# Kernel optimization log

Measured on AMD Instinct MI355X. Metric: run time of the kernel, lower is better.

## Reference

```python
import jax, jax.numpy as jnp
import numpy as np

H = 256  # hidden_size


def _lstm_layer(x, W_ih, W_hh, b_ih, b_hh):
    """Single LSTM layer, batch_first input x: [B, T, I]. PyTorch gate order i,f,g,o."""
    # Precompute input contribution for all timesteps: [B, T, 4H]
    gx = jnp.einsum('bti,gi->btg', x, W_ih) + (b_ih + b_hh)
    gx = jnp.swapaxes(gx, 0, 1)  # [T, B, 4H]
    B = x.shape[0]
    h0 = jnp.zeros((B, H), dtype=x.dtype)
    c0 = jnp.zeros((B, H), dtype=x.dtype)

    def step(carry, g_t):
        h, c = carry
        g = g_t + h @ W_hh.T  # [B, 4H]
        i, f, gg, o = jnp.split(g, 4, axis=-1)
        i = jax.nn.sigmoid(i)
        f = jax.nn.sigmoid(f)
        gg = jnp.tanh(gg)
        o = jax.nn.sigmoid(o)
        c_new = f * c + i * gg
        h_new = o * jnp.tanh(c_new)
        return (h_new, c_new), h_new

    _, hs = jax.lax.scan(step, (h0, c0), gx)  # hs: [T, B, H]
    return jnp.swapaxes(hs, 0, 1)  # [B, T, H]


def setup_inputs() -> dict:
    key = jax.random.key(0)
    ks = jax.random.split(key, 12)
    B, T, I = 512, 256, 10
    s_in = 1.0 / np.sqrt(H)
    inp = {
        'x': jax.random.normal(ks[0], (B, T, I), dtype=jnp.float32),
        # layer 0: input_size=10
        'W_ih0': jax.random.uniform(ks[1], (4 * H, I), jnp.float32, -s_in, s_in),
        'W_hh0': jax.random.uniform(ks[2], (4 * H, H), jnp.float32, -s_in, s_in),
        'b_ih0': jax.random.uniform(ks[3], (4 * H,), jnp.float32, -s_in, s_in),
        'b_hh0': jax.random.uniform(ks[4], (4 * H,), jnp.float32, -s_in, s_in),
        # layer 1: input_size=H
        'W_ih1': jax.random.uniform(ks[5], (4 * H, H), jnp.float32, -s_in, s_in),
        'W_hh1': jax.random.uniform(ks[6], (4 * H, H), jnp.float32, -s_in, s_in),
        'b_ih1': jax.random.uniform(ks[7], (4 * H,), jnp.float32, -s_in, s_in),
        'b_hh1': jax.random.uniform(ks[8], (4 * H,), jnp.float32, -s_in, s_in),
        # final linear head: hidden_size -> 1
        'W_lin': jax.random.uniform(ks[9], (1, H), jnp.float32, -s_in, s_in),
        'b_lin': jax.random.uniform(ks[10], (1,), jnp.float32, -s_in, s_in),
    }
    return inp


def reference(x, W_ih0, W_hh0, b_ih0, b_hh0, W_ih1, W_hh1, b_ih1, b_hh1, W_lin, b_lin):
    h1 = _lstm_layer(x, W_ih0, W_hh0, b_ih0, b_hh0)   # [B, T, H]
    h2 = _lstm_layer(h1, W_ih1, W_hh1, b_ih1, b_hh1)  # [B, T, H]
    y = h2[:, -1, :] @ W_lin.T + b_lin                # [B, 1]
    return y
```

## Files before the change

kernel.cpp:

```cpp
#include <hip/hip_runtime.h>
#include <math.h>

typedef unsigned int u32;
typedef unsigned long long u64;
typedef __attribute__((ext_vector_type(8))) short bf16x8;
typedef __attribute__((ext_vector_type(4))) float f32x4;
typedef __attribute__((ext_vector_type(4))) int i32x4;

#define TT 256

#define BOFF_WT   0ULL
#define BOFF_WX   3932160ULL
#define BOFF_H0HI 3973120ULL
#define BOFF_H0LO 4497408ULL
#define BOFF_H1HI 5021696ULL
#define BOFF_H1LO 5545984ULL
#define BOFF_FLG  6070272ULL

#define OB_H0HI 3973120u
#define OB_H0LO 4497408u
#define OB_H1HI 5021696u
#define OB_H1LO 5545984u
#define OB_FLGF 6070272u
#define OB_FLGS 6074368u

__global__ void transpose_gi(const float* __restrict__ W, float* __restrict__ A, int K) {
    int idx = blockIdx.x * 256 + threadIdx.x;
    if (idx < K * 1024) {
        int kk = idx >> 10, r = idx & 1023, k = r >> 2, g = r & 3;
        A[idx] = W[(g * 256 + k) * K + kk];
    }
}

__global__ void split_w(const float* __restrict__ W0, const float* __restrict__ W1,
                        const float* __restrict__ W2, unsigned short* __restrict__ wt) {
    int idx = blockIdx.x * 256 + threadIdx.x;
    int k32 = idx & 31;
    int n   = (idx >> 5) & 1023;
    int kc  = (idx >> 15) & 7;
    int mt  = idx >> 18;
    const float* W = (mt == 0) ? W0 : (mt == 1) ? W1 : W2;
    int ug = n >> 2, g = n & 3, k = kc * 32 + k32;
    float v = W[(g * 256 + ug) * 256 + k];
    u32 b = __float_as_uint(v);
    unsigned short hi = (unsigned short)(b >> 16);
    float lo = v - __uint_as_float(b & 0xFFFF0000u);
    u32 lb = __float_as_uint(lo);
    unsigned short los = (unsigned short)((lb + 0x7FFFu + ((lb >> 16) & 1u)) >> 16);
    wt[((size_t)((mt * 2 + 0) * 8 + kc) * 1024 + n) * 40 + k32] = hi;
    wt[((size_t)((mt * 2 + 1) * 8 + kc) * 1024 + n) * 40 + k32] = los;
}

__device__ __forceinline__ float sigf(float x)     { return 1.0f / (1.0f + __expf(-x)); }
__device__ __forceinline__ float tanhfast(float x) { return 1.0f - 2.0f / (__expf(2.0f * x) + 1.0f); }

__device__ __forceinline__ unsigned short bhi(float v) {
    return (unsigned short)(__float_as_uint(v) >> 16);
}
__device__ __forceinline__ unsigned short blo(float v) {
    float lo = v - __uint_as_float(__float_as_uint(v) & 0xFFFF0000u);
    u32 lb = __float_as_uint(lo);
    return (unsigned short)((lb + 0x7FFFu + ((lb >> 16) & 1u)) >> 16);
}
__device__ __forceinline__ float bff(u32 us) { return __uint_as_float(us << 16); }

__device__ __forceinline__ i32x4 mksrd(const void* p) {
    u64 a = (u64)p;
    i32x4 r;
    r.x = (int)(u32)a;
    r.y = (int)((a >> 32) & 0xFFFFu);
    r.z = (int)0xFFFFFFFFu;
    r.w = 0x00020000;
    return r;
}

#define WAITV(N) do { asm volatile("s_waitcnt vmcnt(" #N ")" ::: "memory"); \
                      __builtin_amdgcn_sched_barrier(0); } while (0)

__device__ __forceinline__ void ld16s(bf16x8& d, i32x4 rs, u32 voff) {
    asm volatile("buffer_load_dwordx4 %0, %1, %2, 0 offen sc0"
                 : "=v"(d) : "v"(voff), "s"(rs));
}
__device__ __forceinline__ void st4s(i32x4 rs, u32 voff, u32 v) {
    asm volatile("buffer_store_dword %0, %1, %2, 0 offen sc0"
                 :: "v"(v), "v"(voff), "s"(rs) : "memory");
}
__device__ __forceinline__ u32 ld4s(i32x4 rs, u32 voff) {
    u32 d;
    asm volatile("buffer_load_dword %0, %1, %2, 0 offen sc0"
                 : "=v"(d) : "v"(voff), "s"(rs) : "memory");
    return d;
}
__device__ __forceinline__ u32 mkrdy_fast(i32x4 rs, u32 flB, int lane, u32 tgt) {
    u32 v;
    u32 off = flB + (u32)((lane & 31) * 4);
    asm volatile("buffer_load_dword %0, %1, %2, 0 offen sc0\n\t"
                 "s_waitcnt vmcnt(0)"
                 : "=v"(v) : "v"(off), "s"(rs) : "memory");
    unsigned long long b = __ballot(v >= tgt);
    return (u32)b;
}
__device__ __forceinline__ u32 mkrdy_safe(const u32* fl, int lane, u32 tgt) {
    u32 v = __hip_atomic_load(fl + (lane & 31), __ATOMIC_RELAXED,
                              __HIP_MEMORY_SCOPE_AGENT);
    unsigned long long b = __ballot(v >= tgt);
    return (u32)b;
}

__global__ __launch_bounds__(256, 1)
void lstm_mfma(const float* __restrict__ x,
               const float* __restrict__ bih0, const float* __restrict__ bhh0,
               const float* __restrict__ bih1, const float* __restrict__ bhh1,
               const float* __restrict__ Wlin, const float* __restrict__ blin,
               char* __restrict__ wsb, float* __restrict__ out)
{
    __shared__ unsigned short lw[61440];
    __shared__ float fsh[5184];
    float* ldsWx = fsh;
    float* xs    = fsh + 320;
    float* CS    = fsh + 960;

    const int tid  = threadIdx.x;
    const int lane = tid & 63;
    const int wv   = __builtin_amdgcn_readfirstlane(tid >> 6);
    const int quad = lane >> 4;
    const int l15  = lane & 15;
    const int ib   = blockIdx.x & 7;
    const int ik   = blockIdx.x >> 3;
    const int rb0  = ib * 64;

    i32x4 rs = mksrd(wsb);

    const unsigned short* wt = (const unsigned short*)(wsb + BOFF_WT);
    const float* gWx = (const float*)(wsb + BOFF_WX);
    const u32 flF  = OB_FLGF + (u32)(ib * 128);
    const u32* flS = (const u32*)(wsb + OB_FLGS) + ib * 32;
    u32* flSw      = (u32*)(wsb + OB_FLGS) + ib * 32 + ik;

    #pragma unroll 1
    for (int j = 0; j < 30; ++j) {
        int i16 = tid + j * 256;
        int chk = i16 / 160;
        int wi  = i16 - chk * 160;
        size_t src = (size_t)chk * 40960 + (size_t)ik * 1280 + (size_t)wi * 8;
        *(ulonglong2*)(lw + (size_t)chk * 1280 + (size_t)wi * 8) =
            *(const ulonglong2*)(wt + src);
    }
    for (int n = tid; n < 320; n += 256)
        ldsWx[n] = gWx[(n >> 5) * 1024 + ik * 32 + (n & 31)];

    float b0r[8], b1r[8];
    {
        int up = tid & 3;
        #pragma unroll
        for (int j = 0; j < 8; ++j) {
            int ul = up * 2 + (j >> 2), g = j & 3;
            int gi = g * 256 + ik * 8 + ul;
            b0r[j] = bih0[gi] + bhh0[gi];
            b1r[j] = bih1[gi] + bhh1[gi];
        }
    }
    float c0s[2] = {0.f, 0.f}, c1s[2] = {0.f, 0.f};
    const u32 oaB = (u32)(quad * 1024 + (wv * 16 + l15) * 16);
    const bf16x8* bw = (const bf16x8*)lw;
    int safeMode = 0;

    __syncthreads();

    for (int e = 0; e <= TT; ++e) {
        {
            int te = (e < TT) ? e : (TT - 1);
            #pragma unroll
            for (int rr = 0; rr < 2; ++rr) {
                int idx = tid + rr * 256;
                if (idx < 320) {
                    int r = idx / 5, j2 = idx - r * 5;
                    float2 v = *(const float2*)(x + (size_t)(rb0 + r) * 2560 + te * 10 + 2 * j2);
                    xs[(2 * j2) * 64 + r]     = v.x;
                    xs[(2 * j2 + 1) * 64 + r] = v.y;
                }
            }
        }
        __syncthreads();

        {
            const u32 tgt = (u32)e;
            u32 rdy;
            if (!safeMode) {
                rdy = mkrdy_fast(rs, flF, lane, tgt);
                int sp = 0;
                while (rdy != 0xFFFFFFFFu && ++sp < 4096)
                    rdy = mkrdy_fast(rs, flF, lane, tgt);
                if (rdy != 0xFFFFFFFFu) safeMode = 1;
            }
            if (safeMode) {
                rdy = mkrdy_safe(flS, lane, tgt);
                while (rdy != 0xFFFFFFFFu) {
                    __builtin_amdgcn_s_sleep(2);
                    rdy = mkrdy_safe(flS, lane, tgt);
                }
            }
            __builtin_amdgcn_sched_barrier(0);
        }
        WAITV(0);

        const u32 vo0 = OB_H0HI + (u32)((((e + 1) & 1) * 8 + ib) * 32768);
        const u32 vo1 = OB_H0LO + (u32)((((e + 1) & 1) * 8 + ib) * 32768);
        const u32 vo2 = OB_H1HI + (u32)(((e & 1) * 8 + ib) * 32768);
        const u32 vo3 = OB_H1LO + (u32)(((e & 1) * 8 + ib) * 32768);

        bf16x8 fA[2][4];
        #define ISSUE(b, qc) { const u32 tB = (u32)((qc) * 4096) + oaB;   \
            ld16s(fA[b][0], rs, vo0 + tB);                                \
            ld16s(fA[b][1], rs, vo1 + tB);                                \
            ld16s(fA[b][2], rs, vo2 + tB);                                \
            ld16s(fA[b][3], rs, vo3 + tB); }
        ISSUE(0, 0)
        ISSUE(1, 1)

        float xc[8];
        {
            int r = tid >> 2, up = tid & 3;
            #pragma unroll
            for (int j = 0; j < 8; ++j) xc[j] = b0r[j];
            #pragma unroll
            for (int i = 0; i < 10; ++i) {
                float xv = xs[i * 64 + r];
                #pragma unroll
                for (int j = 0; j < 8; ++j)
                    xc[j] += xv * ldsWx[i * 32 + up * 8 + j];
            }
        }

        f32x4 C0[2], C1[2];
        #pragma unroll
        for (int ct = 0; ct < 2; ++ct) {
            C0[ct] = (f32x4){0.f, 0.f, 0.f, 0.f};
            C1[ct] = (f32x4){0.f, 0.f, 0.f, 0.f};
        }

        #pragma unroll
        for (int q = 0; q < 8; ++q) {
            const int b = q & 1;
            bf16x8 wA[2][2], wB[2][2], wC[2][2];
            #pragma unroll
            for (int ct = 0; ct < 2; ++ct) {
                int rb = ct * 16 + l15;
                wA[0][ct] = bw[5 * ((0 * 8 + q) * 32 + rb) + quad];
                wA[1][ct] = bw[5 * ((1 * 8 + q) * 32 + rb) + quad];
                wB[0][ct] = bw[5 * ((2 * 8 + q) * 32 + rb) + quad];
                wB[1][ct] = bw[5 * ((3 * 8 + q) * 32 + rb) + quad];
                wC[0][ct] = bw[5 * ((4 * 8 + q) * 32 + rb) + quad];
                wC[1][ct] = bw[5 * ((5 * 8 + q) * 32 + rb) + quad];
            }
            if (q < 7) { WAITV(4); } else { WAITV(0); }
            bf16x8 a0h = fA[b][0], a0l = fA[b][1];
            bf16x8 a1h = fA[b][2], a1l = fA[b][3];
            #pragma unroll
            for (int ct = 0; ct < 2; ++ct) {
                C0[ct] = __builtin_amdgcn_mfma_f32_16x16x32_bf16(a0h, wA[0][ct], C0[ct], 0, 0, 0);
                C0[ct] = __builtin_amdgcn_mfma_f32_16x16x32_bf16(a0h, wA[1][ct], C0[ct], 0, 0, 0);
                C0[ct] = __builtin_amdgcn_mfma_f32_16x16x32_bf16(a0l, wA[0][ct], C0[ct], 0, 0, 0);
                C0[ct] = __builtin_amdgcn_mfma_f32_16x16x32_bf16(a0l, wA[1][ct], C0[ct], 0, 0, 0);
                C1[ct] = __builtin_amdgcn_mfma_f32_16x16x32_bf16(a0h, wB[0][ct], C1[ct], 0, 0, 0);
                C1[ct] = __builtin_amdgcn_mfma_f32_16x16x32_bf16(a0h, wB[1][ct], C1[ct], 0, 0, 0);
                C1[ct] = __builtin_amdgcn_mfma_f32_16x16x32_bf16(a0l, wB[0][ct], C1[ct], 0, 0, 0);
                C1[ct] = __builtin_amdgcn_mfma_f32_16x16x32_bf16(a0l, wB[1][ct], C1[ct], 0, 0, 0);
                C1[ct] = __builtin_amdgcn_mfma_f32_16x16x32_bf16(a1h, wC[0][ct], C1[ct], 0, 0, 0);
                C1[ct] = __builtin_amdgcn_mfma_f32_16x16x32_bf16(a1h, wC[1][ct], C1[ct], 0, 0, 0);
                C1[ct] = __builtin_amdgcn_mfma_f32_16x16x32_bf16(a1l, wC[0][ct], C1[ct], 0, 0, 0);
                C1[ct] = __builtin_amdgcn_mfma_f32_16x16x32_bf16(a1l, wC[1][ct], C1[ct], 0, 0, 0);
            }
            if (q < 6) ISSUE(b, q + 2)
        }
        #undef ISSUE

        #pragma unroll
        for (int ct = 0; ct < 2; ++ct)
            #pragma unroll
            for (int reg = 0; reg < 4; ++reg) {
                int rr = wv * 16 + quad * 4 + reg;
                CS[rr * 33 + ct * 16 + l15]        = C0[ct][reg];
                CS[2112 + rr * 33 + ct * 16 + l15] = C1[ct][reg];
            }
        __syncthreads();

        {
            int r = tid >> 2, up = tid & 3;
            if (e < TT) {
                float h0n[2];
                #pragma unroll
                for (int s = 0; s < 2; ++s) {
                    int c4 = up * 8 + s * 4;
                    float gi = CS[r * 33 + c4 + 0] + xc[s * 4 + 0];
                    float gf = CS[r * 33 + c4 + 1] + xc[s * 4 + 1];
                    float gg = CS[r * 33 + c4 + 2] + xc[s * 4 + 2];
                    float go = CS[r * 33 + c4 + 3] + xc[s * 4 + 3];
                    float cn = sigf(gf) * c0s[s] + sigf(gi) * tanhfast(gg);
                    c0s[s] = cn;
                    h0n[s] = sigf(go) * tanhfast(cn);
                }
                u32 sb = (u32)(((e & 1) * 8 + ib) * 32768 + ik * 1024 + 4 * tid);
                st4s(rs, OB_H0HI + sb, (u32)bhi(h0n[0]) | ((u32)bhi(h0n[1]) << 16));
                st4s(rs, OB_H0LO + sb, (u32)blo(h0n[0]) | ((u32)blo(h0n[1]) << 16));
            }
            if (e > 0) {
                float h1n[2];
                #pragma unroll
                for (int s = 0; s < 2; ++s) {
                    int c4 = up * 8 + s * 4;
                    float gi = CS[2112 + r * 33 + c4 + 0] + b1r[s * 4 + 0];
                    float gf = CS[2112 + r * 33 + c4 + 1] + b1r[s * 4 + 1];
                    float gg = CS[2112 + r * 33 + c4 + 2] + b1r[s * 4 + 2];
                    float go = CS[2112 + r * 33 + c4 + 3] + b1r[s * 4 + 3];
                    float cn = sigf(gf) * c1s[s] + sigf(gi) * tanhfast(gg);
                    c1s[s] = cn;
                    h1n[s] = sigf(go) * tanhfast(cn);
                }
                u32 sb = (u32)((((e + 1) & 1) * 8 + ib) * 32768 + ik * 1024 + 4 * tid);
                st4s(rs, OB_H1HI + sb, (u32)bhi(h1n[0]) | ((u32)bhi(h1n[1]) << 16));
                st4s(rs, OB_H1LO + sb, (u32)blo(h1n[0]) | ((u32)blo(h1n[1]) << 16));
            }
        }
        WAITV(0);
        __syncthreads();
        if (tid == 0) {
            st4s(rs, flF + (u32)(ik * 4), (u32)(e + 1));
            __hip_atomic_store(flSw, (u32)(e + 1),
                               __ATOMIC_RELAXED, __HIP_MEMORY_SCOPE_AGENT);
        }
    }

    if (ik == 0) {
        {
            const u32 tgt = (u32)(TT + 1);
            u32 rdy;
            if (!safeMode) {
                rdy = mkrdy_fast(rs, flF, lane, tgt);
                int sp = 0;
                while (rdy != 0xFFFFFFFFu && ++sp < 4096)
                    rdy = mkrdy_fast(rs, flF, lane, tgt);
                if (rdy != 0xFFFFFFFFu) safeMode = 1;
            }
            if (safeMode) {
                rdy = mkrdy_safe(flS, lane, tgt);
                while (rdy != 0xFFFFFFFFu) {
                    __builtin_amdgcn_s_sleep(2);
                    rdy = mkrdy_safe(flS, lane, tgt);
                }
            }
            __builtin_amdgcn_sched_barrier(0);
        }
        int r = tid >> 2, q4 = tid & 3;
        const u32 bh_ = OB_H1HI + (u32)((8 + ib) * 32768);
        const u32 bl_ = OB_H1LO + (u32)((8 + ib) * 32768);
        float sacc = 0.f;
        #pragma unroll 1
        for (int kk = 0; kk < 64; kk += 8) {
            u32 hw4[4], lw4[4];
            #pragma unroll
            for (int t = 0; t < 4; ++t) {
                int k = q4 * 64 + kk + 2 * t;
                u32 sa = (u32)(((k >> 3) * 512 + r * 8 + (k & 7)) * 2);
                hw4[t] = ld4s(rs, bh_ + sa);
                lw4[t] = ld4s(rs, bl_ + sa);
            }
            WAITV(0);
            #pragma unroll
            for (int t = 0; t < 4; ++t) {
                int k = q4 * 64 + kk + 2 * t;
                sacc += (bff(hw4[t] & 0xFFFFu) + bff(lw4[t] & 0xFFFFu)) * Wlin[k];
                sacc += (bff(hw4[t] >> 16)     + bff(lw4[t] >> 16))     * Wlin[k + 1];
            }
        }
        sacc += __shfl_down(sacc, 2, 4);
        sacc += __shfl_down(sacc, 1, 4);
        if (q4 == 0) out[rb0 + r] = sacc + blin[0];
    }
}

extern "C" void kernel_launch(void* const* d_in, const int* in_sizes, int n_in,
                              void* d_out, int out_size, void* d_ws, size_t ws_size,
                              hipStream_t stream) {
    const float* x     = (const float*)d_in[0];
    const float* W_ih0 = (const float*)d_in[1];
    const float* W_hh0 = (const float*)d_in[2];
    const float* b_ih0 = (const float*)d_in[3];
    const float* b_hh0 = (const float*)d_in[4];
    const float* W_ih1 = (const float*)d_in[5];
    const float* W_hh1 = (const float*)d_in[6];
    const float* b_ih1 = (const float*)d_in[7];
    const float* b_hh1 = (const float*)d_in[8];
    const float* W_lin = (const float*)d_in[9];
    const float* b_lin = (const float*)d_in[10];
    float* out = (float*)d_out;
    char* wsb  = (char*)d_ws;

    hipMemsetAsync(wsb + BOFF_H0HI, 0, 4 * 524288 + 131584, stream);

    split_w<<<3072, 256, 0, stream>>>(W_hh0, W_ih1, W_hh1,
                                      (unsigned short*)(wsb + BOFF_WT));
    transpose_gi<<<40, 256, 0, stream>>>(W_ih0, (float*)(wsb + BOFF_WX), 10);

    lstm_mfma<<<256, 256, 0, stream>>>(x, b_ih0, b_hh0, b_ih1, b_hh1,
                                       W_lin, b_lin, wsb, out);
}
```

Before: 1.546 ms.

## Wait on per-chunk producer readiness bits instead of a full-step barrier

Replaces the single wait for all 32 producer flags at the start of each timestep with incremental waits. Each chunk of the hidden-state K dimension waits only on the flag bits of the blocks that produce that chunk, just before its loads are issued. This lets the MFMA work on early chunks overlap with producers that are still finishing the later chunks. It adds repeated flag polling inside the inner loop and changes the spin limit and sleep interval, which could add overhead or contention.

```diff
diff --git a/kernel.cpp b/kernel.cpp
--- a/kernel.cpp
+++ b/kernel.cpp
@@ -182,27 +182,30 @@
             }
         }
         __syncthreads();
-
-        {
-            const u32 tgt = (u32)e;
-            u32 rdy;
-            if (!safeMode) {
-                rdy = mkrdy_fast(rs, flF, lane, tgt);
-                int sp = 0;
-                while (rdy != 0xFFFFFFFFu && ++sp < 4096)
-                    rdy = mkrdy_fast(rs, flF, lane, tgt);
-                if (rdy != 0xFFFFFFFFu) safeMode = 1;
-            }
-            if (safeMode) {
-                rdy = mkrdy_safe(flS, lane, tgt);
-                while (rdy != 0xFFFFFFFFu) {
-                    __builtin_amdgcn_s_sleep(2);
-                    rdy = mkrdy_safe(flS, lane, tgt);
-                }
-            }
-            __builtin_amdgcn_sched_barrier(0);
-        }
         WAITV(0);
+
+        const u32 tgt = (u32)e;
+        u32 rdy = 0;
+        #define WBITS(mask) do {                                            \
+            if ((rdy & (mask)) != (mask)) {                                 \
+                if (!safeMode) {                                            \
+                    int sp = 0;                                             \
+                    do {                                                    \
+                        rdy = mkrdy_fast(rs, flF, lane, tgt);               \
+                        if ((rdy & (mask)) == (mask)) break;                \
+                    } while (++sp < 8192);                                  \
+                    if ((rdy & (mask)) != (mask)) safeMode = 1;             \
+                }                                                           \
+                if (safeMode) {                                             \
+                    rdy = mkrdy_safe(flS, lane, tgt);                       \
+                    while ((rdy & (mask)) != (mask)) {                      \
+                        __builtin_amdgcn_s_sleep(1);                        \
+                        rdy = mkrdy_safe(flS, lane, tgt);                   \
+                    }                                                       \
+                }                                                           \
+                __builtin_amdgcn_sched_barrier(0);                          \
+            }                                                               \
+        } while (0)
 
         const u32 vo0 = OB_H0HI + (u32)((((e + 1) & 1) * 8 + ib) * 32768);
         const u32 vo1 = OB_H0LO + (u32)((((e + 1) & 1) * 8 + ib) * 32768);
@@ -215,6 +218,7 @@
             ld16s(fA[b][1], rs, vo1 + tB);                                \
             ld16s(fA[b][2], rs, vo2 + tB);                                \
             ld16s(fA[b][3], rs, vo3 + tB); }
+        WBITS(0x000000FFu);
         ISSUE(0, 0)
         ISSUE(1, 1)
 
@@ -271,9 +275,18 @@
                 C1[ct] = __builtin_amdgcn_mfma_f32_16x16x32_bf16(a1l, wC[0][ct], C1[ct], 0, 0, 0);
                 C1[ct] = __builtin_amdgcn_mfma_f32_16x16x32_bf16(a1l, wC[1][ct], C1[ct], 0, 0, 0);
             }
-            if (q < 6) ISSUE(b, q + 2)
+            if (q < 6) {
+                if (q == 0)      WBITS(0x00000F00u);
+                else if (q == 1) WBITS(0x0000F000u);
+                else if (q == 2) WBITS(0x000F0000u);
+                else if (q == 3) WBITS(0x00F00000u);
+                else if (q == 4) WBITS(0x0F000000u);
+                else             WBITS(0xF0000000u);
+                ISSUE(b, q + 2)
+            }
         }
         #undef ISSUE
+        #undef WBITS
 
         #pragma unroll
         for (int ct = 0; ct < 2; ++ct)
@@ -338,7 +351,7 @@
             if (!safeMode) {
                 rdy = mkrdy_fast(rs, flF, lane, tgt);
                 int sp = 0;
-                while (rdy != 0xFFFFFFFFu && ++sp < 4096)
+                while (rdy != 0xFFFFFFFFu && ++sp < 8192)
                     rdy = mkrdy_fast(rs, flF, lane, tgt);
                 if (rdy != 0xFFFFFFFFu) safeMode = 1;
             }
```

After: 1.897 ms. 22.7% more time.
